# Kernel optimization log

Measured on AMD Instinct MI355X. Metric: run time of the kernel, lower is better.

The kernel has to match this reference:

```python
import jax, jax.numpy as jnp
import numpy as np

EMBED_DIM = 512
N_HEAD = 8
Q_DIM = 64
V_DIM = 64
WINDOW_SIZE = 3


def setup_inputs() -> dict:
    key = jax.random.key(0)
    ks = jax.random.split(key, 9)
    B, N = 2, 2048
    x = jax.random.normal(ks[0], (B, N, EMBED_DIM), dtype=jnp.float32)
    s = 0.02
    # torch nn.Linear weights are [out_features, in_features]; y = x @ W.T + b
    Wq = jax.random.normal(ks[1], (N_HEAD * Q_DIM, EMBED_DIM), dtype=jnp.float32) * s
    bq = jax.random.normal(ks[2], (N_HEAD * Q_DIM,), dtype=jnp.float32) * s
    Wk = jax.random.normal(ks[3], (N_HEAD * Q_DIM, EMBED_DIM), dtype=jnp.float32) * s
    bk = jax.random.normal(ks[4], (N_HEAD * Q_DIM,), dtype=jnp.float32) * s
    Wv = jax.random.normal(ks[5], (N_HEAD * V_DIM, EMBED_DIM), dtype=jnp.float32) * s
    bv = jax.random.normal(ks[6], (N_HEAD * V_DIM,), dtype=jnp.float32) * s
    Wo = jax.random.normal(ks[7], (EMBED_DIM, N_HEAD * V_DIM), dtype=jnp.float32) * s
    bo = jax.random.normal(ks[8], (EMBED_DIM,), dtype=jnp.float32) * s
    return {"x": x, "Wq": Wq, "bq": bq, "Wk": Wk, "bk": bk,
            "Wv": Wv, "bv": bv, "Wo": Wo, "bo": bo}


def _diag_indices(n_seq, di):
    # rows i and cols j = i + di of the di-th diagonal
    if di >= 0:
        ii = np.arange(0, n_seq - di)
    else:
        ii = np.arange(-di, n_seq)
    return ii, ii + di


def reference(x, Wq, bq, Wk, bk, Wv, bv, Wo, bo):
    B, N, E = x.shape
    H, Dq, Dv = N_HEAD, Q_DIM, V_DIM
    Q = (x @ Wq.T + bq).reshape(B, N, H, Dq).transpose(0, 2, 1, 3)  # [B,H,N,Dq]
    K = (x @ Wk.T + bk).reshape(B, N, H, Dq).transpose(0, 2, 1, 3)
    V = (x @ Wv.T + bv).reshape(B, N, H, Dv).transpose(0, 2, 1, 3)  # [B,H,N,Dv]
    half = WINDOW_SIZE // 2
    # Faithful to source: scores scattered into COLUMN index i (the loop
    # counter), not the key position; all other columns remain 0 and still
    # participate in the full softmax over n_seq.
    columns = jnp.zeros((B, H, N, N), dtype=x.dtype)
    for i, di in enumerate(range(-half, half + 1)):
        ii, jj = _diag_indices(N, di)
        c = jnp.einsum('bhid,bhid->bhi', Q[:, :, ii, :], K[:, :, jj, :])
        columns = columns.at[:, :, ii, i].set(c)
    attn = jax.nn.softmax(columns, axis=-1)          # [B,H,N,N]
    out = attn @ V                                    # [B,H,N,Dv]
    out = out.transpose(0, 2, 1, 3).reshape(B, N, H * Dv)
    return out @ Wo.T + bo
```

## Files before the change

### kernel.cpp

```cpp
#include <hip/hip_runtime.h>
#include <hip/hip_bf16.h>

#define EMBED 512
#define NSEQ 2048
#define NROWS 4096
#define QKV_STRIDE 1536

typedef unsigned short u16;
typedef __bf16 bf16x8 __attribute__((ext_vector_type(8)));
typedef float f32x4 __attribute__((ext_vector_type(4)));

__device__ __forceinline__ u16 f2bf(float f) {
    unsigned u = __float_as_uint(f);
    unsigned r = (u + 0x7FFFu + ((u >> 16) & 1u)) >> 16;
    return (u16)r;
}

#define XELEMS    (NROWS * EMBED)
#define WCATELEMS (1536 * EMBED)
#define NCONVB    1408

__global__ __launch_bounds__(256) void prep_kernel(
    const float* __restrict__ x,
    const float* __restrict__ Wq, const float* __restrict__ Wk,
    const float* __restrict__ Wv, const float* __restrict__ bv,
    u16* __restrict__ xb, u16* __restrict__ Wcat, float* __restrict__ vs)
{
    if (blockIdx.x == NCONVB) {
#pragma unroll
        for (int i = 0; i < 4; ++i) {
            const int idx = threadIdx.x + i * 256;
            vs[idx] = (float)NSEQ * bv[idx & 511];
        }
        return;
    }
    const long long e0 = (long long)(blockIdx.x * 256 + threadIdx.x) * 8;
    const float* src;
    u16* dst;
    if (e0 < XELEMS) {
        src = x + e0; dst = xb + e0;
    } else {
        const long long j = e0 - XELEMS;
        const int row = (int)(j >> 9);
        const int col = (int)(j & 511);
        const int sel = row >> 9;
        const int r   = row & 511;
        const float* W = (sel == 0) ? Wq : (sel == 1) ? Wk : Wv;
        src = W + (size_t)r * EMBED + col; dst = Wcat + j;
    }
    float4 a = *(const float4*)(src);
    float4 b = *(const float4*)(src + 4);
    union { u16 u[8]; uint4 v; } p;
    p.u[0] = f2bf(a.x); p.u[1] = f2bf(a.y); p.u[2] = f2bf(a.z); p.u[3] = f2bf(a.w);
    p.u[4] = f2bf(b.x); p.u[5] = f2bf(b.y); p.u[6] = f2bf(b.z); p.u[7] = f2bf(b.w);
    *(uint4*)(dst) = p.v;
}

__global__ __launch_bounds__(256) void gemm_qkv_mfma(
    const u16* __restrict__ A, const u16* __restrict__ W,
    const float* __restrict__ bq, const float* __restrict__ bk,
    const float* __restrict__ bvv, float* __restrict__ QKV,
    float* __restrict__ vs)
{
    __shared__ __align__(16) u16 As[128 * 64];
    __shared__ __align__(16) u16 Bs[64 * 64];

    const int m0 = (blockIdx.x & 31) * 128;
    const int n0 = (blockIdx.x >> 5) * 64;
    const int sel = n0 >> 9;
    const float* bias = ((sel == 0) ? bq : (sel == 1) ? bk : bvv) + (n0 & 511);

    const int t    = threadIdx.x;
    const int wave = t >> 6, lane = t & 63;
    const int wm   = wave >> 1, wn = wave & 1;
    const int qd   = lane >> 4, lr = lane & 15;

    const int sr8 = lane >> 3;
    const int sg  = (lane & 7) ^ sr8;
    const int soff = sg * 8;

    f32x4 acc[4][2] = {};

    const u16* Ag = A + (size_t)m0 * EMBED;
    const u16* Wg = W + (size_t)n0 * EMBED;

    u16* Adst = As + (size_t)(wave * 8) * 64;
    u16* Bdst = Bs + (size_t)(wave * 8) * 64;
    const u16* Asrc = Ag + (size_t)(wave * 8 + sr8) * EMBED + soff;
    const u16* Bsrc = Wg + (size_t)(wave * 8 + sr8) * EMBED + soff;

    for (int kc = 0; kc < EMBED; kc += 64) {
#pragma unroll
        for (int j = 0; j < 4; ++j)
            __builtin_amdgcn_global_load_lds(
                (const __attribute__((address_space(1))) void*)(Asrc + kc + (size_t)j * 32 * EMBED),
                (__attribute__((address_space(3))) void*)(Adst + j * 32 * 64), 16, 0, 0);
#pragma unroll
        for (int j = 0; j < 2; ++j)
            __builtin_amdgcn_global_load_lds(
                (const __attribute__((address_space(1))) void*)(Bsrc + kc + (size_t)j * 32 * EMBED),
                (__attribute__((address_space(3))) void*)(Bdst + j * 32 * 64), 16, 0, 0);
        __syncthreads();

#pragma unroll
        for (int kk = 0; kk < 2; ++kk) {
            const int gr = ((kk * 4 + qd) ^ (lr & 7)) * 8;
            bf16x8 af[4], bfr[2];
#pragma unroll
            for (int i = 0; i < 4; ++i)
                af[i]  = *(const bf16x8*)&As[(wm * 64 + i * 16 + lr) * 64 + gr];
#pragma unroll
            for (int i = 0; i < 2; ++i)
                bfr[i] = *(const bf16x8*)&Bs[(wn * 32 + i * 16 + lr) * 64 + gr];
#pragma unroll
            for (int mi = 0; mi < 4; ++mi)
#pragma unroll
                for (int ni = 0; ni < 2; ++ni)
                    acc[mi][ni] = __builtin_amdgcn_mfma_f32_16x16x32_bf16(
                        af[mi], bfr[ni], acc[mi][ni], 0, 0, 0);
        }
        __syncthreads();
    }

    if (sel < 2) {
#pragma unroll
        for (int ni = 0; ni < 2; ++ni) {
            const int cl = wn * 32 + ni * 16 + lr;
            const float bb = bias[cl];
#pragma unroll
            for (int mi = 0; mi < 4; ++mi)
#pragma unroll
                for (int e = 0; e < 4; ++e) {
                    const int row = m0 + wm * 64 + mi * 16 + qd * 4 + e;
                    QKV[(size_t)row * QKV_STRIDE + n0 + cl] = acc[mi][ni][e] + bb;
                }
        }
    } else {
        const int batch = m0 >> 11;
#pragma unroll
        for (int ni = 0; ni < 2; ++ni) {
            const int cl  = wn * 32 + ni * 16 + lr;
            const int col = n0 + cl;
            const float bb = bias[cl];
            float s = 0.f;
#pragma unroll
            for (int mi = 0; mi < 4; ++mi)
#pragma unroll
                for (int e = 0; e < 4; ++e) {
                    const int row = m0 + wm * 64 + mi * 16 + qd * 4 + e;
                    s += acc[mi][ni][e];
                    if ((row & (NSEQ - 1)) < 3)
                        QKV[(size_t)row * QKV_STRIDE + col] = acc[mi][ni][e] + bb;
                }
            s += __shfl_xor(s, 16);
            s += __shfl_xor(s, 32);
            if (qd == 0)
                atomicAdd(&vs[batch * 512 + (col - 1024)], s);
        }
    }
}

__global__ __launch_bounds__(256) void wsmall_kernel(
    const float* __restrict__ QKV, const float* __restrict__ vs,
    const float* __restrict__ Wo, float* __restrict__ WT)
{
    __shared__ float Vsm[4][512];
    const int b  = blockIdx.x >> 6;
    const int jb = blockIdx.x & 63;
    const int t  = threadIdx.x;

    const float* Vbase = QKV + (size_t)b * NSEQ * QKV_STRIDE + 1024;
    for (int idx = t; idx < 512; idx += 256) {
        const float v0 = Vbase[idx];
        const float v1 = Vbase[QKV_STRIDE + idx];
        const float v2 = Vbase[2 * QKV_STRIDE + idx];
        Vsm[0][idx] = v0; Vsm[1][idx] = v1; Vsm[2][idx] = v2;
        Vsm[3][idx] = vs[b * 512 + idx] - (v0 + v1 + v2);
    }
    __syncthreads();

    const int j  = jb * 8 + (t >> 5);
    const int s  = t & 31;
    const int h  = s >> 2, tt = s & 3;
    const float* Wor = Wo + (size_t)j * EMBED + h * 64;
    const float* vr  = &Vsm[tt][h * 64];
    float acc = 0.f;
#pragma unroll
    for (int c = 0; c < 64; ++c) {
        const int cc = (c + 2 * s) & 63;
        acc = fmaf(vr[cc], Wor[cc], acc);
    }
    WT[((size_t)b * 512 + j) * 32 + s] = acc;
}

__global__ __launch_bounds__(256) void attn_out_kernel(
    const float* __restrict__ QKV, const float* __restrict__ WT,
    const float* __restrict__ bo, float* __restrict__ out)
{
    __shared__ float E[16][32];
    const int r0   = blockIdx.x * 16;
    const int b    = r0 >> 11;
    const int wave = threadIdx.x >> 6, lane = threadIdx.x & 63;
    const int d0   = lane * 8;

#pragma unroll
    for (int i = 0; i < 4; ++i) {
        const int rl = wave * 4 + i;
        const int r  = r0 + rl;
        const int sr = r & (NSEQ - 1);
        const float* Qr = QKV + (size_t)r * QKV_STRIDE + d0;
        const float* Kr = QKV + (size_t)r * QKV_STRIDE + 512 + d0;

        float4 qa = *(const float4*)(Qr);
        float4 qb = *(const float4*)(Qr + 4);
        float4 ka = *(const float4*)(Kr);
        float4 kb = *(const float4*)(Kr + 4);
        float s1 = qa.x*ka.x + qa.y*ka.y + qa.z*ka.z + qa.w*ka.w
                 + qb.x*kb.x + qb.y*kb.y + qb.z*kb.z + qb.w*kb.w;
        float s0 = 0.f, s2 = 0.f;
        if (sr > 0) {
            float4 pa = *(const float4*)(Kr - QKV_STRIDE);
            float4 pb = *(const float4*)(Kr - QKV_STRIDE + 4);
            s0 = qa.x*pa.x + qa.y*pa.y + qa.z*pa.z + qa.w*pa.w
               + qb.x*pb.x + qb.y*pb.y + qb.z*pb.z + qb.w*pb.w;
        }
        if (sr < NSEQ - 1) {
            float4 na = *(const float4*)(Kr + QKV_STRIDE);
            float4 nb = *(const float4*)(Kr + QKV_STRIDE + 4);
            s2 = qa.x*na.x + qa.y*na.y + qa.z*na.z + qa.w*na.w
               + qb.x*nb.x + qb.y*nb.y + qb.z*nb.z + qb.w*nb.w;
        }
#pragma unroll
        for (int off = 1; off <= 4; off <<= 1) {
            s0 += __shfl_xor(s0, off);
            s1 += __shfl_xor(s1, off);
            s2 += __shfl_xor(s2, off);
        }
        const float m  = fmaxf(fmaxf(s0, s1), fmaxf(s2, 0.f));
        const float e0 = __expf(s0 - m);
        const float e1 = __expf(s1 - m);
        const float e2 = __expf(s2 - m);
        const float eb = __expf(-m);
        const float rd = 1.f / (e0 + e1 + e2 + (float)(NSEQ - 3) * eb);
        const int h = lane >> 3, jj = lane & 7;
        const float coef = (jj == 0) ? e0 : (jj == 1) ? e1 : (jj == 2) ? e2 : eb;
        if (jj < 4) E[rl][h * 4 + jj] = coef * rd;
    }
    __syncthreads();

    const int j0 = threadIdx.x * 2;
    const float* WTb = WT + (size_t)b * 512 * 32;
    float w0[32], w1[32];
#pragma unroll
    for (int s = 0; s < 32; ++s) {
        w0[s] = WTb[(size_t)j0 * 32 + s];
        w1[s] = WTb[(size_t)(j0 + 1) * 32 + s];
    }
    const float b0 = bo[j0], b1 = bo[j0 + 1];
#pragma unroll
    for (int rl = 0; rl < 16; ++rl) {
        float a0 = b0, a1 = b1;
#pragma unroll
        for (int s = 0; s < 32; ++s) {
            const float e = E[rl][s];
            a0 = fmaf(e, w0[s], a0);
            a1 = fmaf(e, w1[s], a1);
        }
        float2 o = make_float2(a0, a1);
        *(float2*)(out + (size_t)(r0 + rl) * EMBED + j0) = o;
    }
}

extern "C" void kernel_launch(void* const* d_in, const int* in_sizes, int n_in,
                              void* d_out, int out_size, void* d_ws, size_t ws_size,
                              hipStream_t stream)
{
    const float* x  = (const float*)d_in[0];
    const float* Wq = (const float*)d_in[1];
    const float* bq = (const float*)d_in[2];
    const float* Wk = (const float*)d_in[3];
    const float* bk = (const float*)d_in[4];
    const float* Wv = (const float*)d_in[5];
    const float* bv = (const float*)d_in[6];
    const float* Wo = (const float*)d_in[7];
    const float* bo = (const float*)d_in[8];
    float* out = (float*)d_out;

    float* QKV  = (float*)d_ws;
    u16*   xb   = (u16*)(QKV + (size_t)NROWS * QKV_STRIDE);
    u16*   Wcat = xb + XELEMS;
    float* vs   = (float*)(Wcat + WCATELEMS);
    float* WT   = vs + 1024;

    prep_kernel<<<NCONVB + 1, 256, 0, stream>>>(x, Wq, Wk, Wv, bv, xb, Wcat, vs);
    gemm_qkv_mfma<<<768, 256, 0, stream>>>(xb, Wcat, bq, bk, bv, QKV, vs);
    wsmall_kernel<<<128, 256, 0, stream>>>(QKV, vs, Wo, WT);
    attn_out_kernel<<<256, 256, 0, stream>>>(QKV, WT, bo, out);
}
```

Baseline: 107.9 us.

## Store Q/K in bf16, compact V head rows, replace V-sum atomics with partials

The QKV GEMM now writes Q and K as bf16 into a compact 1024-wide buffer instead of fp32 with stride 1536. Only the first three V rows per batch go to a small Vhead buffer, and the column sums of V are written as per-tile partials instead of atomicAdd. The wsmall kernel reduces those partials and adds the N*bv bias term itself, so the extra prep block is removed. This halves the traffic for writing and reading Q/K and drops atomic contention, at the cost of bf16 rounding on Q and K before the window dot products.

```diff
diff --git a/kernel.cpp b/kernel.cpp
--- a/kernel.cpp
+++ b/kernel.cpp
@@ -4,17 +4,20 @@
 #define EMBED 512
 #define NSEQ 2048
 #define NROWS 4096
-#define QKV_STRIDE 1536
 
 typedef unsigned short u16;
 typedef __bf16 bf16x8 __attribute__((ext_vector_type(8)));
 typedef float f32x4 __attribute__((ext_vector_type(4)));
+typedef unsigned short ushort8 __attribute__((ext_vector_type(8)));
 
 __device__ __forceinline__ u16 f2bf(float f) {
     unsigned u = __float_as_uint(f);
     unsigned r = (u + 0x7FFFu + ((u >> 16) & 1u)) >> 16;
     return (u16)r;
 }
+__device__ __forceinline__ float bf2f(u16 v) {
+    return __uint_as_float((unsigned)v << 16);
+}
 
 #define XELEMS    (NROWS * EMBED)
 #define WCATELEMS (1536 * EMBED)
@@ -23,17 +26,9 @@
 __global__ __launch_bounds__(256) void prep_kernel(
     const float* __restrict__ x,
     const float* __restrict__ Wq, const float* __restrict__ Wk,
-    const float* __restrict__ Wv, const float* __restrict__ bv,
-    u16* __restrict__ xb, u16* __restrict__ Wcat, float* __restrict__ vs)
-{
-    if (blockIdx.x == NCONVB) {
-#pragma unroll
-        for (int i = 0; i < 4; ++i) {
-            const int idx = threadIdx.x + i * 256;
-            vs[idx] = (float)NSEQ * bv[idx & 511];
-        }
-        return;
-    }
+    const float* __restrict__ Wv,
+    u16* __restrict__ xb, u16* __restrict__ Wcat)
+{
     const long long e0 = (long long)(blockIdx.x * 256 + threadIdx.x) * 8;
     const float* src;
     u16* dst;
@@ -59,8 +54,9 @@
 __global__ __launch_bounds__(256) void gemm_qkv_mfma(
     const u16* __restrict__ A, const u16* __restrict__ W,
     const float* __restrict__ bq, const float* __restrict__ bk,
-    const float* __restrict__ bvv, float* __restrict__ QKV,
-    float* __restrict__ vs)
+    const float* __restrict__ bvv,
+    u16* __restrict__ QKb, float* __restrict__ Vhead,
+    float* __restrict__ vpart)
 {
     __shared__ __align__(16) u16 As[128 * 64];
     __shared__ __align__(16) u16 Bs[64 * 64];
@@ -132,15 +128,16 @@
 #pragma unroll
                 for (int e = 0; e < 4; ++e) {
                     const int row = m0 + wm * 64 + mi * 16 + qd * 4 + e;
-                    QKV[(size_t)row * QKV_STRIDE + n0 + cl] = acc[mi][ni][e] + bb;
+                    QKb[(size_t)row * 1024 + n0 + cl] = f2bf(acc[mi][ni][e] + bb);
                 }
         }
     } else {
         const int batch = m0 >> 11;
+        const int mtb   = (m0 >> 7) & 15;
 #pragma unroll
         for (int ni = 0; ni < 2; ++ni) {
             const int cl  = wn * 32 + ni * 16 + lr;
-            const int col = n0 + cl;
+            const int col = (n0 - 1024) + cl;
             const float bb = bias[cl];
             float s = 0.f;
 #pragma unroll
@@ -150,18 +147,20 @@
                     const int row = m0 + wm * 64 + mi * 16 + qd * 4 + e;
                     s += acc[mi][ni][e];
                     if ((row & (NSEQ - 1)) < 3)
-                        QKV[(size_t)row * QKV_STRIDE + col] = acc[mi][ni][e] + bb;
+                        Vhead[(size_t)batch * 1536 + (row & (NSEQ - 1)) * 512 + col]
+                            = acc[mi][ni][e] + bb;
                 }
             s += __shfl_xor(s, 16);
             s += __shfl_xor(s, 32);
             if (qd == 0)
-                atomicAdd(&vs[batch * 512 + (col - 1024)], s);
+                vpart[((size_t)batch * 512 + col) * 32 + mtb * 2 + wm] = s;
         }
     }
 }
 
 __global__ __launch_bounds__(256) void wsmall_kernel(
-    const float* __restrict__ QKV, const float* __restrict__ vs,
+    const float* __restrict__ Vhead, const float* __restrict__ vpart,
+    const float* __restrict__ bv,
     const float* __restrict__ Wo, float* __restrict__ WT)
 {
     __shared__ float Vsm[4][512];
@@ -169,13 +168,16 @@
     const int jb = blockIdx.x & 63;
     const int t  = threadIdx.x;
 
-    const float* Vbase = QKV + (size_t)b * NSEQ * QKV_STRIDE + 1024;
     for (int idx = t; idx < 512; idx += 256) {
-        const float v0 = Vbase[idx];
-        const float v1 = Vbase[QKV_STRIDE + idx];
-        const float v2 = Vbase[2 * QKV_STRIDE + idx];
+        const float v0 = Vhead[(size_t)b * 1536 + idx];
+        const float v1 = Vhead[(size_t)b * 1536 + 512 + idx];
+        const float v2 = Vhead[(size_t)b * 1536 + 1024 + idx];
+        float sum = 0.f;
+        const float* vp = vpart + ((size_t)b * 512 + idx) * 32;
+#pragma unroll
+        for (int s = 0; s < 32; ++s) sum += vp[s];
         Vsm[0][idx] = v0; Vsm[1][idx] = v1; Vsm[2][idx] = v2;
-        Vsm[3][idx] = vs[b * 512 + idx] - (v0 + v1 + v2);
+        Vsm[3][idx] = sum + (float)NSEQ * bv[idx] - (v0 + v1 + v2);
     }
     __syncthreads();
 
@@ -194,7 +196,7 @@
 }
 
 __global__ __launch_bounds__(256) void attn_out_kernel(
-    const float* __restrict__ QKV, const float* __restrict__ WT,
+    const u16* __restrict__ QKb, const float* __restrict__ WT,
     const float* __restrict__ bo, float* __restrict__ out)
 {
     __shared__ float E[16][32];
@@ -208,27 +210,29 @@
         const int rl = wave * 4 + i;
         const int r  = r0 + rl;
         const int sr = r & (NSEQ - 1);
-        const float* Qr = QKV + (size_t)r * QKV_STRIDE + d0;
-        const float* Kr = QKV + (size_t)r * QKV_STRIDE + 512 + d0;
-
-        float4 qa = *(const float4*)(Qr);
-        float4 qb = *(const float4*)(Qr + 4);
-        float4 ka = *(const float4*)(Kr);
-        float4 kb = *(const float4*)(Kr + 4);
-        float s1 = qa.x*ka.x + qa.y*ka.y + qa.z*ka.z + qa.w*ka.w
-                 + qb.x*kb.x + qb.y*kb.y + qb.z*kb.z + qb.w*kb.w;
+        const u16* Qr = QKb + (size_t)r * 1024 + d0;
+        const u16* Kr = QKb + (size_t)r * 1024 + 512 + d0;
+
+        ushort8 qv = *(const ushort8*)Qr;
+        ushort8 kv = *(const ushort8*)Kr;
+        float q[8], k[8];
+#pragma unroll
+        for (int z = 0; z < 8; ++z) { q[z] = bf2f(qv[z]); k[z] = bf2f(kv[z]); }
+
+        float s1 = 0.f;
+#pragma unroll
+        for (int z = 0; z < 8; ++z) s1 = fmaf(q[z], k[z], s1);
+
         float s0 = 0.f, s2 = 0.f;
         if (sr > 0) {
-            float4 pa = *(const float4*)(Kr - QKV_STRIDE);
-            float4 pb = *(const float4*)(Kr - QKV_STRIDE + 4);
-            s0 = qa.x*pa.x + qa.y*pa.y + qa.z*pa.z + qa.w*pa.w
-               + qb.x*pb.x + qb.y*pb.y + qb.z*pb.z + qb.w*pb.w;
+            ushort8 pv = *(const ushort8*)(Kr - 1024);
+#pragma unroll
+            for (int z = 0; z < 8; ++z) s0 = fmaf(q[z], bf2f(pv[z]), s0);
         }
         if (sr < NSEQ - 1) {
-            float4 na = *(const float4*)(Kr + QKV_STRIDE);
-            float4 nb = *(const float4*)(Kr + QKV_STRIDE + 4);
-            s2 = qa.x*na.x + qa.y*na.y + qa.z*na.z + qa.w*na.w
-               + qb.x*nb.x + qb.y*nb.y + qb.z*nb.z + qb.w*nb.w;
+            ushort8 nv = *(const ushort8*)(Kr + 1024);
+#pragma unroll
+            for (int z = 0; z < 8; ++z) s2 = fmaf(q[z], bf2f(nv[z]), s2);
         }
 #pragma unroll
         for (int off = 1; off <= 4; off <<= 1) {
@@ -286,14 +290,15 @@
     const float* bo = (const float*)d_in[8];
     float* out = (float*)d_out;
 
-    float* QKV  = (float*)d_ws;
-    u16*   xb   = (u16*)(QKV + (size_t)NROWS * QKV_STRIDE);
-    u16*   Wcat = xb + XELEMS;
-    float* vs   = (float*)(Wcat + WCATELEMS);
-    float* WT   = vs + 1024;
-
-    prep_kernel<<<NCONVB + 1, 256, 0, stream>>>(x, Wq, Wk, Wv, bv, xb, Wcat, vs);
-    gemm_qkv_mfma<<<768, 256, 0, stream>>>(xb, Wcat, bq, bk, bv, QKV, vs);
-    wsmall_kernel<<<128, 256, 0, stream>>>(QKV, vs, Wo, WT);
-    attn_out_kernel<<<256, 256, 0, stream>>>(QKV, WT, bo, out);
-}
+    u16*   QKb   = (u16*)d_ws;
+    u16*   xb    = QKb + (size_t)NROWS * 1024;
+    u16*   Wcat  = xb + XELEMS;
+    float* Vhead = (float*)(Wcat + WCATELEMS);
+    float* vpart = Vhead + 2 * 3 * 512;
+    float* WT    = vpart + 2 * 512 * 32;
+
+    prep_kernel<<<NCONVB, 256, 0, stream>>>(x, Wq, Wk, Wv, xb, Wcat);
+    gemm_qkv_mfma<<<768, 256, 0, stream>>>(xb, Wcat, bq, bk, bv, QKb, Vhead, vpart);
+    wsmall_kernel<<<128, 256, 0, stream>>>(Vhead, vpart, bv, Wo, WT);
+    attn_out_kernel<<<256, 256, 0, stream>>>(QKb, WT, bo, out);
+}
```

Result: faster. 105.5 us (-2.2%).
